# Optimization experiments

Measured on AMD Instinct MI355X. Metric: run time of the kernel, lower is better.

The kernel has to match this reference:

```python
import jax, jax.numpy as jnp
import numpy as np

N = 500000   # candidates
C = 128      # field centers
D = 64       # latent dim
EPS = 1e-6
TEMP = 0.1
DT = 0.1


def setup_inputs() -> dict:
    key = jax.random.key(0)
    k1, k2, k3, k4 = jax.random.split(key, 4)
    query_z = jax.random.normal(k1, (1, D), dtype=jnp.float32)
    candidate_z = jax.random.normal(k2, (N, D), dtype=jnp.float32)
    centers = jax.random.normal(k3, (C, D), dtype=jnp.float32)
    mus = jax.random.uniform(k4, (C,), dtype=jnp.float32) * 0.5 + 0.1  # positive masses
    return {"query_z": query_z, "candidate_z": candidate_z, "centers": centers, "mus": mus}


def _cdist(a, b):
    # Euclidean distance matrix (|a|^2 + |b|^2 - 2 a.b)^(1/2), clamped for stability
    d2 = (jnp.sum(a * a, axis=-1, keepdims=True)
          + jnp.sum(b * b, axis=-1)[None, :]
          - 2.0 * (a @ b.T))
    return jnp.sqrt(jnp.maximum(d2, 1e-12))


def _potential(z, centers, mus):
    # pot_i = sum_j mu_j / (dist(z_i, c_j) + eps)   -> (len(z),)
    d = _cdist(z, centers)                      # (B, C)
    return jnp.sum(mus[None, :] / (d + EPS), axis=1)


def _pm_field(z, centers, mus):
    # Gravitational flow step: z + dt * sum_j mu_j * (c_j - z) / (r^3 + eps)
    diff = centers[None, :, :] - z[:, None, :]          # (B, C, D)
    r = jnp.sqrt(jnp.maximum(jnp.sum(diff * diff, axis=-1, keepdims=True), 1e-12))
    return z + DT * jnp.sum(mus[None, :, None] * diff / (r ** 3 + EPS), axis=1)


def reference(query_z, candidate_z, centers, mus):
    query_output = _pm_field(query_z, centers, mus)        # (1, D)
    q_pot = _potential(query_z, centers, mus)              # (1,)
    c_pot = _potential(candidate_z, centers, mus)          # (N,)
    logits = -jnp.abs(q_pot - c_pot) / TEMP                # (N,)
    attention = jax.nn.softmax(logits, axis=0)             # (N,)
    return query_output, attention
```

## Files before the change

### kernel.cpp

```cpp
#include <hip/hip_runtime.h>
#include <hip/hip_bf16.h>

#define N_CAND     500000
#define N_PAIRS    15625
#define INV_TEMP   10.0f
#define DT_STEP    0.1f
#define POT_BLOCKS 1024

typedef __attribute__((ext_vector_type(8))) short  short8;
typedef __attribute__((ext_vector_type(4))) float  floatx4;

__device__ inline short f32_to_bf16_rne(float f) {
    unsigned u = __builtin_bit_cast(unsigned, f);
    u += 0x7FFFu + ((u >> 16) & 1u);
    return (short)(u >> 16);
}

__device__ inline void cvt8v(floatx4 v0, floatx4 v1, short8& b, float& ss) {
#pragma unroll
    for (int k = 0; k < 4; ++k) {
        ss = fmaf(v0[k], v0[k], ss);
        ss = fmaf(v1[k], v1[k], ss);
        b[k]     = f32_to_bf16_rne(v0[k]);
        b[k + 4] = f32_to_bf16_rne(v1[k]);
    }
}

__global__ __launch_bounds__(256)
void pot_kernel(const float* __restrict__ qz, const float* __restrict__ cand,
                const float* __restrict__ centers, const float* __restrict__ mus,
                float* __restrict__ out, float* __restrict__ partials) {
    __shared__ __align__(16) short8  cfrag[8][2][64];
    __shared__ __align__(16) floatx4 ncin[8][4];
    __shared__ __align__(16) floatx4 muv8[8][4];
    __shared__ float qred[4], sred[4], wj[128];

    int tid = threadIdx.x, wid = tid >> 6, lane = tid & 63;
    int lr = lane & 15;
    int lg = lane >> 4;

    {
        int j = tid >> 1;
        int h = tid & 1;
        const float* crow = centers + j * 64 + h * 32;
        const float* qrow = qz + h * 32;
        float ssd = 0.f;
#pragma unroll
        for (int k = 0; k < 8; ++k) {
            floatx4 c4 = *(const floatx4*)(crow + k * 4);
            floatx4 q4 = *(const floatx4*)(qrow + k * 4);
#pragma unroll
            for (int x = 0; x < 4; ++x) { float df = c4[x] - q4[x]; ssd = fmaf(df, df, ssd); }
        }
        ssd += __shfl_xor(ssd, 1);
        float rs = __builtin_amdgcn_rsqf(fmaxf(ssd, 1e-12f));
        float mu_j = mus[j];
        float potj = (h == 0) ? mu_j * rs : 0.f;
        if (blockIdx.x == 0 && h == 0)
            wj[j] = mu_j * rs * rs * rs;
#pragma unroll
        for (int m = 1; m < 64; m <<= 1) potj += __shfl_xor(potj, m);
        if (lane == 0) qred[wid] = potj;
    }

#pragma unroll
    for (int c2 = 0; c2 < 2; ++c2) {
        int ct = wid * 2 + c2;
        int j = ct * 16 + lr;
        const float* p = centers + j * 64 + lg * 8;
        float ncp = 0.f;
        short8 b0, b1;
        cvt8v(*(const floatx4*)p,        *(const floatx4*)(p + 4),  b0, ncp);
        cvt8v(*(const floatx4*)(p + 32), *(const floatx4*)(p + 36), b1, ncp);
        cfrag[ct][0][lane] = b0;
        cfrag[ct][1][lane] = b1;
        ncp += __shfl_xor(ncp, 16);
        ncp += __shfl_xor(ncp, 32);
        if (lg == 0) ((float*)ncin)[ct * 16 + lr] = -0.5f * ncp;
        if (lg == 1) ((float*)muv8)[ct * 16 + lr] = mus[j];
    }
    __syncthreads();
    float q_pot = qred[0] + qred[1] + qred[2] + qred[3];

    if (blockIdx.x == 0 && tid < 64) {
        float qd = qz[tid];
        float acc = 0.f;
        for (int jj = 0; jj < 128; ++jj)
            acc = fmaf(wj[jj], centers[jj * 64 + tid] - qd, acc);
        out[tid] = fmaf(DT_STEP, acc, qd);
    }

    float lsum = 0.f;
    const float* baseA = cand + (size_t)lr * 64 + lg * 8;
    for (int p = blockIdx.x * 4 + wid; p < N_PAIRS; p += POT_BLOCKS * 4) {
        size_t r0 = (size_t)p * 32;
        const float* pa = baseA + r0 * 64;
        const float* pb = pa + 16 * 64;
        floatx4 a0 = *(const floatx4*)pa;
        floatx4 a1 = *(const floatx4*)(pa + 4);
        floatx4 a2 = *(const floatx4*)(pa + 32);
        floatx4 a3 = *(const floatx4*)(pa + 36);
        floatx4 c0 = *(const floatx4*)pb;
        floatx4 c1 = *(const floatx4*)(pb + 4);
        floatx4 c2 = *(const floatx4*)(pb + 32);
        floatx4 c3 = *(const floatx4*)(pb + 36);

        short8 afA[2], afB[2];
        float nzA = 0.f, nzB = 0.f;
        cvt8v(a0, a1, afA[0], nzA);
        cvt8v(a2, a3, afA[1], nzA);
        cvt8v(c0, c1, afB[0], nzB);
        cvt8v(c2, c3, afB[1], nzB);
        nzA += __shfl_xor(nzA, 16);
        nzA += __shfl_xor(nzA, 32);
        nzB += __shfl_xor(nzB, 16);
        nzB += __shfl_xor(nzB, 32);

        float potA = 0.f, potB = 0.f;
#pragma unroll
        for (int ct = 0; ct < 8; ++ct) {
            floatx4 nci = ncin[ct][lg];
            floatx4 m4  = muv8[ct][lg];
            short8 f0 = cfrag[ct][0][lane];
            short8 f1 = cfrag[ct][1][lane];
            floatx4 aA = __builtin_amdgcn_mfma_f32_16x16x32_bf16(f0, afA[0], nci, 0, 0, 0);
            aA         = __builtin_amdgcn_mfma_f32_16x16x32_bf16(f1, afA[1], aA,  0, 0, 0);
            floatx4 aB = __builtin_amdgcn_mfma_f32_16x16x32_bf16(f0, afB[0], nci, 0, 0, 0);
            aB         = __builtin_amdgcn_mfma_f32_16x16x32_bf16(f1, afB[1], aB,  0, 0, 0);
#pragma unroll
            for (int r = 0; r < 4; ++r) {
                float d2A = fmaxf(fmaf(-2.f, aA[r], nzA), 1e-12f);
                potA = fmaf(m4[r], __builtin_amdgcn_rsqf(d2A), potA);
                float d2B = fmaxf(fmaf(-2.f, aB[r], nzB), 1e-12f);
                potB = fmaf(m4[r], __builtin_amdgcn_rsqf(d2B), potB);
            }
        }
        potA += __shfl_xor(potA, 16);
        potA += __shfl_xor(potA, 32);
        potB += __shfl_xor(potB, 16);
        potB += __shfl_xor(potB, 32);

        if (lg == 0) {
            float eA = __expf(-fabsf(q_pot - potA) * INV_TEMP);
            float eB = __expf(-fabsf(q_pot - potB) * INV_TEMP);
            out[64 + r0 + lr]      = eA;
            out[64 + r0 + 16 + lr] = eB;
            lsum += eA + eB;
        }
    }

#pragma unroll
    for (int m = 1; m < 64; m <<= 1) lsum += __shfl_xor(lsum, m);
    if (lane == 0) sred[wid] = lsum;
    __syncthreads();
    if (tid == 0) partials[blockIdx.x] = sred[0] + sred[1] + sred[2] + sred[3];
}

__global__ __launch_bounds__(256)
void norm_kernel(float* __restrict__ att, const float* __restrict__ partials) {
    int tid = threadIdx.x;
    float p = partials[tid] + partials[tid + 256] + partials[tid + 512] + partials[tid + 768];
#pragma unroll
    for (int m = 1; m < 64; m <<= 1) p += __shfl_xor(p, m);
    __shared__ float red[4];
    if ((tid & 63) == 0) red[tid >> 6] = p;
    __syncthreads();
    float inv = 1.0f / (red[0] + red[1] + red[2] + red[3]);
    int i = blockIdx.x * 256 + tid;
    if (i < N_CAND / 4) {
        floatx4 v = *(floatx4*)(att + (size_t)i * 4);
#pragma unroll
        for (int k = 0; k < 4; ++k) v[k] *= inv;
        *(floatx4*)(att + (size_t)i * 4) = v;
    }
}

extern "C" void kernel_launch(void* const* d_in, const int* in_sizes, int n_in,
                              void* d_out, int out_size, void* d_ws, size_t ws_size,
                              hipStream_t stream) {
    const float* qz   = (const float*)d_in[0];
    const float* cand = (const float*)d_in[1];
    const float* ctr  = (const float*)d_in[2];
    const float* mus  = (const float*)d_in[3];
    float* out = (float*)d_out;
    float* ws  = (float*)d_ws;

    pot_kernel<<<POT_BLOCKS, 256, 0, stream>>>(qz, cand, ctr, mus, out, ws + 256);
    int blocks2 = (N_CAND / 4 + 255) / 256;
    norm_kernel<<<blocks2, 256, 0, stream>>>(out + 64, ws + 256);
}
```

Before: 42.58 us.

## Prefetch next candidate tile and use truncating bf16 pack via perm

Software-pipelines the candidate loop so the next pair's global loads are issued before the current pair's MFMA and rsqrt work, hiding memory latency. Replaces the round-to-nearest bf16 conversion with a single byte-permute truncation per pair of floats, removes the d2 clamp, switches exp to exp2 with a folded constant, and adds an occupancy hint to launch_bounds. Truncation changes rounding of the distances slightly, and dropping the clamp risks NaN or inf if d2 goes non-positive. Holding the prefetched vectors raises register pressure.

Measured after the change: 115.6 us. 172% more time.

```diff
diff --git a/kernel.cpp b/kernel.cpp
--- a/kernel.cpp
+++ b/kernel.cpp
@@ -3,30 +3,33 @@
 
 #define N_CAND     500000
 #define N_PAIRS    15625
-#define INV_TEMP   10.0f
+#define IT_LOG2E   14.426950408889634f
 #define DT_STEP    0.1f
 #define POT_BLOCKS 1024
+#define STRIDE     (POT_BLOCKS * 4)
 
 typedef __attribute__((ext_vector_type(8))) short  short8;
 typedef __attribute__((ext_vector_type(4))) float  floatx4;
+typedef __attribute__((ext_vector_type(4))) unsigned int uintx4;
 
-__device__ inline short f32_to_bf16_rne(float f) {
-    unsigned u = __builtin_bit_cast(unsigned, f);
-    u += 0x7FFFu + ((u >> 16) & 1u);
-    return (short)(u >> 16);
+__device__ inline unsigned pk(float lo, float hi) {
+    return __builtin_amdgcn_perm(__builtin_bit_cast(unsigned, hi),
+                                 __builtin_bit_cast(unsigned, lo), 0x07060302u);
 }
 
-__device__ inline void cvt8v(floatx4 v0, floatx4 v1, short8& b, float& ss) {
+__device__ inline short8 pack8(floatx4 v0, floatx4 v1, float& ss) {
+    uintx4 w;
+    w[0] = pk(v0[0], v0[1]); w[1] = pk(v0[2], v0[3]);
+    w[2] = pk(v1[0], v1[1]); w[3] = pk(v1[2], v1[3]);
 #pragma unroll
     for (int k = 0; k < 4; ++k) {
         ss = fmaf(v0[k], v0[k], ss);
         ss = fmaf(v1[k], v1[k], ss);
-        b[k]     = f32_to_bf16_rne(v0[k]);
-        b[k + 4] = f32_to_bf16_rne(v1[k]);
     }
+    return __builtin_bit_cast(short8, w);
 }
 
-__global__ __launch_bounds__(256)
+__global__ __launch_bounds__(256, 4)
 void pot_kernel(const float* __restrict__ qz, const float* __restrict__ cand,
                 const float* __restrict__ centers, const float* __restrict__ mus,
                 float* __restrict__ out, float* __restrict__ partials) {
@@ -69,9 +72,8 @@
         int j = ct * 16 + lr;
         const float* p = centers + j * 64 + lg * 8;
         float ncp = 0.f;
-        short8 b0, b1;
-        cvt8v(*(const floatx4*)p,        *(const floatx4*)(p + 4),  b0, ncp);
-        cvt8v(*(const floatx4*)(p + 32), *(const floatx4*)(p + 36), b1, ncp);
+        short8 b0 = pack8(*(const floatx4*)p,        *(const floatx4*)(p + 4),  ncp);
+        short8 b1 = pack8(*(const floatx4*)(p + 32), *(const floatx4*)(p + 36), ncp);
         cfrag[ct][0][lane] = b0;
         cfrag[ct][1][lane] = b1;
         ncp += __shfl_xor(ncp, 16);
@@ -92,29 +94,26 @@
 
     float lsum = 0.f;
     const float* baseA = cand + (size_t)lr * 64 + lg * 8;
-    for (int p = blockIdx.x * 4 + wid; p < N_PAIRS; p += POT_BLOCKS * 4) {
+    floatx4 v0, v1, v2, v3, v4, v5, v6, v7;
+#define LOADP(pp) { const float* pa = baseA + (size_t)(pp) * 2048;          \
+        v0 = *(const floatx4*)pa;        v1 = *(const floatx4*)(pa + 4);    \
+        v2 = *(const floatx4*)(pa + 32); v3 = *(const floatx4*)(pa + 36);   \
+        const float* pb = pa + 1024;                                        \
+        v4 = *(const floatx4*)pb;        v5 = *(const floatx4*)(pb + 4);    \
+        v6 = *(const floatx4*)(pb + 32); v7 = *(const floatx4*)(pb + 36); }
+
+    int p = blockIdx.x * 4 + wid;
+    LOADP(p);
+    while (p < N_PAIRS) {
+        float nzA = 0.f, nzB = 0.f;
+        short8 afA0 = pack8(v0, v1, nzA), afA1 = pack8(v2, v3, nzA);
+        short8 afB0 = pack8(v4, v5, nzB), afB1 = pack8(v6, v7, nzB);
         size_t r0 = (size_t)p * 32;
-        const float* pa = baseA + r0 * 64;
-        const float* pb = pa + 16 * 64;
-        floatx4 a0 = *(const floatx4*)pa;
-        floatx4 a1 = *(const floatx4*)(pa + 4);
-        floatx4 a2 = *(const floatx4*)(pa + 32);
-        floatx4 a3 = *(const floatx4*)(pa + 36);
-        floatx4 c0 = *(const floatx4*)pb;
-        floatx4 c1 = *(const floatx4*)(pb + 4);
-        floatx4 c2 = *(const floatx4*)(pb + 32);
-        floatx4 c3 = *(const floatx4*)(pb + 36);
+        p += STRIDE;
+        if (p < N_PAIRS) LOADP(p);
 
-        short8 afA[2], afB[2];
-        float nzA = 0.f, nzB = 0.f;
-        cvt8v(a0, a1, afA[0], nzA);
-        cvt8v(a2, a3, afA[1], nzA);
-        cvt8v(c0, c1, afB[0], nzB);
-        cvt8v(c2, c3, afB[1], nzB);
-        nzA += __shfl_xor(nzA, 16);
-        nzA += __shfl_xor(nzA, 32);
-        nzB += __shfl_xor(nzB, 16);
-        nzB += __shfl_xor(nzB, 32);
+        nzA += __shfl_xor(nzA, 16); nzA += __shfl_xor(nzA, 32);
+        nzB += __shfl_xor(nzB, 16); nzB += __shfl_xor(nzB, 32);
 
         float potA = 0.f, potB = 0.f;
 #pragma unroll
@@ -123,31 +122,28 @@
             floatx4 m4  = muv8[ct][lg];
             short8 f0 = cfrag[ct][0][lane];
             short8 f1 = cfrag[ct][1][lane];
-            floatx4 aA = __builtin_amdgcn_mfma_f32_16x16x32_bf16(f0, afA[0], nci, 0, 0, 0);
-            aA         = __builtin_amdgcn_mfma_f32_16x16x32_bf16(f1, afA[1], aA,  0, 0, 0);
-            floatx4 aB = __builtin_amdgcn_mfma_f32_16x16x32_bf16(f0, afB[0], nci, 0, 0, 0);
-            aB         = __builtin_amdgcn_mfma_f32_16x16x32_bf16(f1, afB[1], aB,  0, 0, 0);
+            floatx4 aA = __builtin_amdgcn_mfma_f32_16x16x32_bf16(f0, afA0, nci, 0, 0, 0);
+            aA         = __builtin_amdgcn_mfma_f32_16x16x32_bf16(f1, afA1, aA,  0, 0, 0);
+            floatx4 aB = __builtin_amdgcn_mfma_f32_16x16x32_bf16(f0, afB0, nci, 0, 0, 0);
+            aB         = __builtin_amdgcn_mfma_f32_16x16x32_bf16(f1, afB1, aB,  0, 0, 0);
 #pragma unroll
             for (int r = 0; r < 4; ++r) {
-                float d2A = fmaxf(fmaf(-2.f, aA[r], nzA), 1e-12f);
-                potA = fmaf(m4[r], __builtin_amdgcn_rsqf(d2A), potA);
-                float d2B = fmaxf(fmaf(-2.f, aB[r], nzB), 1e-12f);
-                potB = fmaf(m4[r], __builtin_amdgcn_rsqf(d2B), potB);
+                potA = fmaf(m4[r], __builtin_amdgcn_rsqf(fmaf(-2.f, aA[r], nzA)), potA);
+                potB = fmaf(m4[r], __builtin_amdgcn_rsqf(fmaf(-2.f, aB[r], nzB)), potB);
             }
         }
-        potA += __shfl_xor(potA, 16);
-        potA += __shfl_xor(potA, 32);
-        potB += __shfl_xor(potB, 16);
-        potB += __shfl_xor(potB, 32);
+        potA += __shfl_xor(potA, 16); potA += __shfl_xor(potA, 32);
+        potB += __shfl_xor(potB, 16); potB += __shfl_xor(potB, 32);
 
         if (lg == 0) {
-            float eA = __expf(-fabsf(q_pot - potA) * INV_TEMP);
-            float eB = __expf(-fabsf(q_pot - potB) * INV_TEMP);
+            float eA = exp2f(-IT_LOG2E * fabsf(q_pot - potA));
+            float eB = exp2f(-IT_LOG2E * fabsf(q_pot - potB));
             out[64 + r0 + lr]      = eA;
             out[64 + r0 + 16 + lr] = eB;
             lsum += eA + eB;
         }
     }
+#undef LOADP
 
 #pragma unroll
     for (int m = 1; m < 64; m <<= 1) lsum += __shfl_xor(lsum, m);
```
